# Optimization experiments

Measured on AMD Instinct MI355X. Metric: run time of the kernel, lower is better.

The kernel has to match this reference:

```python
import jax, jax.numpy as jnp
import numpy as np

EPS = 1e-12  # tf.nn.l2_normalize epsilon


def setup_inputs() -> dict:
    key = jax.random.key(0)
    k1, k2, k3 = jax.random.split(key, 3)
    T, NC, FW = 16384, 2048, 100
    x = jax.random.normal(k1, (T, NC), dtype=jnp.float32)
    weights = jax.random.normal(k2, (FW, NC), dtype=jnp.float32)
    biases = jax.random.normal(k3, (1, NC), dtype=jnp.float32)
    return {"x": x, "weights": weights, "biases": biases}


def reference(x, weights, biases):
    # x: [T, NC] (batch_size is the time axis), weights: [FW, NC], biases: [1, NC]
    FW, NC = weights.shape
    # pos_constraint then L2-normalize each filter along the lag axis
    w = jnp.maximum(weights, 0.0)
    w = w * jax.lax.rsqrt(jnp.maximum(jnp.sum(w * w, axis=0, keepdims=True), EPS))
    # The original pads the filter with FW trailing zeros and runs a SAME conv2d
    # over a [NC, T, 1, 1] input, then takes diag_part to recover the per-channel
    # result. With kernel size 2*FW, SAME pads (FW-1) above / FW below; the FW
    # trailing zero taps never contribute, so this equals a cross-correlation
    # with left padding FW-1: out[t, c] = sum_k w[k, c] * x[t + k - (FW-1), c].
    xT = x.T[None]                 # [1, NC, T]
    kern = w.T[:, None, :]         # [NC, 1, FW] depthwise kernel (OIH)
    pre = jax.lax.conv_general_dilated(
        xT, kern,
        window_strides=(1,),
        padding=[(FW - 1, 0)],
        dimension_numbers=("NCH", "OIH", "NCH"),
        feature_group_count=NC,
    )                              # [1, NC, T]
    pre = pre[0].T + biases        # [T, NC]
    return pre  # activation_func='lin' -> identity
```

## Files before the change

### kernel.cpp

```cpp
#include <hip/hip_runtime.h>


#define T_TOT 16384
#define NCH   2048
#define FW    100
#define CB    32
#define TB    128
#define RING  256
#define MROWS 24
#define BROWS (RING + MROWS)
#define NTHR  256
#define TTH   16
#define UK    10
#define NKC   (FW / UK)
#define NSEG  12
#define NCHUNK_TOT (T_TOT / TB)

__global__ __launch_bounds__(NTHR)
void catent_fir(const float* __restrict__ x,
                const float* __restrict__ wraw,
                const float* __restrict__ bias,
                float* __restrict__ out) {
    __shared__ float ring[BROWS * CB];
    __shared__ float wlds[FW * CB];
    __shared__ float scl[CB];

    const int tid   = threadIdx.x;
    const int cgrp  = blockIdx.x & 63;
    const int sidx  = blockIdx.x >> 6;
    const int cbase = cgrp * CB;

    const int ch0 = (sidx * NCHUNK_TOT) / NSEG;
    const int ch1 = ((sidx + 1) * NCHUNK_TOT) / NSEG;
    const int tseg0 = ch0 * TB;

    for (int i = tid; i < FW * CB; i += NTHR) {
        int k = i >> 5, c = i & 31;
        wlds[i] = fmaxf(wraw[(size_t)k * NCH + cbase + c], 0.0f);
    }
    __syncthreads();
    if (tid < CB) {
        float s = 0.0f;
        #pragma unroll 4
        for (int k = 0; k < FW; ++k) { float v = wlds[k * CB + tid]; s = fmaf(v, v, s); }
        scl[tid] = rsqrtf(fmaxf(s, 1e-12f));
    }
    __syncthreads();
    for (int i = tid; i < FW * CB; i += NTHR) wlds[i] *= scl[i & 31];

    for (int p = 0; p < 8; ++p) {
        int idx = tid + p * NTHR;
        int row = idx >> 3;
        int c4  = (idx & 7) * 4;
        int t   = tseg0 - TB + row;
        float4 v = make_float4(0.f, 0.f, 0.f, 0.f);
        if (t >= 0) v = *reinterpret_cast<const float4*>(&x[(size_t)t * NCH + cbase + c4]);
        int r = t & (RING - 1);
        *reinterpret_cast<float4*>(&ring[r * CB + c4]) = v;
        if (r < MROWS)
            *reinterpret_cast<float4*>(&ring[(RING + r) * CB + c4]) = v;
    }
    __syncthreads();

    const int c = tid & 31;
    const int g = tid >> 5;
    const float biasr = bias[cbase + c];

    const int r0  = tid >> 3;
    const int sc4 = (tid & 7) * 4;

    for (int ch = ch0; ch < ch1; ++ch) {
        const int t0 = ch * TB;
        const bool do_stage = (ch + 1 < ch1);

        float4 st[4];
        if (do_stage) {
            const size_t gb = (size_t)(t0 + TB) * NCH + cbase + sc4;
            #pragma unroll
            for (int p = 0; p < 4; ++p)
                st[p] = *reinterpret_cast<const float4*>(&x[gb + (size_t)(r0 + p * 32) * NCH]);
        }

        float acc[TTH];
        #pragma unroll
        for (int i = 0; i < TTH; ++i) acc[i] = biasr;

        const int rowbase0 = t0 - (FW - 1) + g * TTH;
        #pragma unroll 1
        for (int kc = 0; kc < NKC; ++kc) {
            const int br = (rowbase0 + kc * UK) & (RING - 1);
            const float* xb = &ring[br * CB + c];
            const float* wb = &wlds[(kc * UK) * CB + c];
            float wk[UK];
            #pragma unroll
            for (int u = 0; u < UK; ++u) wk[u] = wb[u * CB];
            float xj[TTH + UK - 1];
            #pragma unroll
            for (int j = 0; j < TTH + UK - 1; ++j) xj[j] = xb[j * CB];
            #pragma unroll
            for (int u = 0; u < UK; ++u)
                #pragma unroll
                for (int t = 0; t < TTH; ++t)
                    acc[t] = fmaf(wk[u], xj[t + u], acc[t]);
        }

        {
            size_t ob = (size_t)(t0 + g * TTH) * NCH + cbase + c;
            #pragma unroll
            for (int t = 0; t < TTH; ++t) out[ob + (size_t)t * NCH] = acc[t];
        }

        __syncthreads();

        if (do_stage) {
            const int rbase = (t0 + TB) & (RING - 1);
            #pragma unroll
            for (int p = 0; p < 4; ++p) {
                int r = rbase + r0 + p * 32;
                *reinterpret_cast<float4*>(&ring[r * CB + sc4]) = st[p];
                if (r < MROWS)
                    *reinterpret_cast<float4*>(&ring[(RING + r) * CB + sc4]) = st[p];
            }
        }
        __syncthreads();
    }
}

extern "C" void kernel_launch(void* const* d_in, const int* in_sizes, int n_in,
                              void* d_out, int out_size, void* d_ws, size_t ws_size,
                              hipStream_t stream) {
    const float* x    = (const float*)d_in[0];
    const float* wraw = (const float*)d_in[1];
    const float* bias = (const float*)d_in[2];
    float* out = (float*)d_out;

    dim3 grid(64 * NSEG);
    dim3 block(NTHR);
    catent_fir<<<grid, block, 0, stream>>>(x, wraw, bias, out);
}
```

Before: 130.1 us.

## Transpose LDS ring to channel-major rows with float4 reads and rotating register window

Stores the x ring buffer and weights in LDS as channel-major rows (padded row lengths 292/108) so each thread reads its channel's time samples with float4 loads. The tap loop becomes a rotating 24-entry register window, one 8-tap phase at a time, so each 8 new samples are reused across 16 outputs. Weights get a leading zero pad so the taps line up with 8-aligned sample reads, and output stores move after the staging barrier. In exchange, the global loads for staging become scalar per-channel loads instead of float4, and register pressure rises.

Result: faster. 111.6 us (-14.2%).

```diff
diff --git a/kernel.cpp b/kernel.cpp
--- a/kernel.cpp
+++ b/kernel.cpp
@@ -6,23 +6,40 @@
 #define FW    100
 #define CB    32
 #define TB    128
-#define RING  256
-#define MROWS 24
-#define BROWS (RING + MROWS)
 #define NTHR  256
 #define TTH   16
-#define UK    10
-#define NKC   (FW / UK)
+#define ROWL  292
+#define WROW  108
 #define NSEG  12
 #define NCHUNK_TOT (T_TOT / TB)
+
+#define KC_PHASE(PH, NS) do {                                                   \
+    int ro_ = tk & 255;                                                         \
+    float4 n0_ = *(const float4*)(rrow + ro_);                                  \
+    float4 n1_ = *(const float4*)(rrow + ro_ + 4);                              \
+    float4 w0_ = *(const float4*)(wp);                                          \
+    float4 w1_ = *(const float4*)(wp + 4);                                      \
+    float wk_[8];                                                               \
+    wk_[0]=w0_.x; wk_[1]=w0_.y; wk_[2]=w0_.z; wk_[3]=w0_.w;                     \
+    wk_[4]=w1_.x; wk_[5]=w1_.y; wk_[6]=w1_.z; wk_[7]=w1_.w;                     \
+    xw[(NS)+0]=n0_.x; xw[(NS)+1]=n0_.y; xw[(NS)+2]=n0_.z; xw[(NS)+3]=n0_.w;     \
+    xw[(NS)+4]=n1_.x; xw[(NS)+5]=n1_.y; xw[(NS)+6]=n1_.z; xw[(NS)+7]=n1_.w;     \
+    _Pragma("unroll")                                                           \
+    for (int u_ = 0; u_ < 8; ++u_) {                                            \
+      _Pragma("unroll")                                                         \
+      for (int i_ = 0; i_ < 16; ++i_)                                           \
+        acc[i_] = fmaf(wk_[u_], xw[((PH) + u_ + i_) % 24], acc[i_]);            \
+    }                                                                           \
+    tk += 8; wp += 8;                                                           \
+} while (0)
 
 __global__ __launch_bounds__(NTHR)
 void catent_fir(const float* __restrict__ x,
                 const float* __restrict__ wraw,
                 const float* __restrict__ bias,
                 float* __restrict__ out) {
-    __shared__ float ring[BROWS * CB];
-    __shared__ float wlds[FW * CB];
+    __shared__ float ring[CB * ROWL];
+    __shared__ float wl[CB * WROW];
     __shared__ float scl[CB];
 
     const int tid   = threadIdx.x;
@@ -34,95 +51,125 @@
     const int ch1 = ((sidx + 1) * NCHUNK_TOT) / NSEG;
     const int tseg0 = ch0 * TB;
 
+    const int c = tid & 31;
+    const int g = tid >> 5;
+
     for (int i = tid; i < FW * CB; i += NTHR) {
-        int k = i >> 5, c = i & 31;
-        wlds[i] = fmaxf(wraw[(size_t)k * NCH + cbase + c], 0.0f);
+        int k = i >> 5, cc = i & 31;
+        wl[cc * WROW + k + 1] = fmaxf(wraw[(size_t)k * NCH + cbase + cc], 0.0f);
+    }
+    if (tid < CB) {
+        wl[tid * WROW + 0] = 0.0f;
+        for (int j = FW + 1; j < WROW; ++j) wl[tid * WROW + j] = 0.0f;
     }
     __syncthreads();
     if (tid < CB) {
         float s = 0.0f;
         #pragma unroll 4
-        for (int k = 0; k < FW; ++k) { float v = wlds[k * CB + tid]; s = fmaf(v, v, s); }
+        for (int k = 1; k <= FW; ++k) { float v = wl[tid * WROW + k]; s = fmaf(v, v, s); }
         scl[tid] = rsqrtf(fmaxf(s, 1e-12f));
     }
     __syncthreads();
-    for (int i = tid; i < FW * CB; i += NTHR) wlds[i] *= scl[i & 31];
+    for (int i = tid; i < FW * CB; i += NTHR) {
+        int k = i >> 5, cc = i & 31;
+        wl[cc * WROW + k + 1] *= scl[cc];
+    }
 
-    for (int p = 0; p < 8; ++p) {
-        int idx = tid + p * NTHR;
-        int row = idx >> 3;
-        int c4  = (idx & 7) * 4;
-        int t   = tseg0 - TB + row;
-        float4 v = make_float4(0.f, 0.f, 0.f, 0.f);
-        if (t >= 0) v = *reinterpret_cast<const float4*>(&x[(size_t)t * NCH + cbase + c4]);
-        int r = t & (RING - 1);
-        *reinterpret_cast<float4*>(&ring[r * CB + c4]) = v;
-        if (r < MROWS)
-            *reinterpret_cast<float4*>(&ring[(RING + r) * CB + c4]) = v;
+    {
+        float* rw = &ring[c * ROWL];
+        for (int p = 0; p < 2; ++p) {
+            int tbase = tseg0 - TB + p * TB + g * 16;
+            float v[16];
+            #pragma unroll
+            for (int j = 0; j < 16; ++j) {
+                int t = tbase + j;
+                v[j] = (t >= 0) ? x[(size_t)t * NCH + cbase + c] : 0.0f;
+            }
+            int rm = tbase & 255;
+            #pragma unroll
+            for (int q = 0; q < 4; ++q)
+                *(float4*)(rw + rm + q * 4) = make_float4(v[q*4], v[q*4+1], v[q*4+2], v[q*4+3]);
+            if (rm < 32) {
+                #pragma unroll
+                for (int q = 0; q < 4; ++q)
+                    *(float4*)(rw + 256 + rm + q * 4) = make_float4(v[q*4], v[q*4+1], v[q*4+2], v[q*4+3]);
+            }
+        }
     }
     __syncthreads();
 
-    const int c = tid & 31;
-    const int g = tid >> 5;
     const float biasr = bias[cbase + c];
-
-    const int r0  = tid >> 3;
-    const int sc4 = (tid & 7) * 4;
+    const float* rrow = &ring[c * ROWL];
+    const float* wrow = &wl[c * WROW];
+    float* rwr = &ring[c * ROWL];
 
     for (int ch = ch0; ch < ch1; ++ch) {
         const int t0 = ch * TB;
         const bool do_stage = (ch + 1 < ch1);
 
-        float4 st[4];
+        float stv[16];
         if (do_stage) {
-            const size_t gb = (size_t)(t0 + TB) * NCH + cbase + sc4;
+            const size_t gb = (size_t)(t0 + TB + g * 16) * NCH + cbase + c;
             #pragma unroll
-            for (int p = 0; p < 4; ++p)
-                st[p] = *reinterpret_cast<const float4*>(&x[gb + (size_t)(r0 + p * 32) * NCH]);
+            for (int j = 0; j < 16; ++j) stv[j] = x[gb + (size_t)j * NCH];
         }
 
-        float acc[TTH];
+        float acc[16];
         #pragma unroll
-        for (int i = 0; i < TTH; ++i) acc[i] = biasr;
+        for (int i = 0; i < 16; ++i) acc[i] = biasr;
 
-        const int rowbase0 = t0 - (FW - 1) + g * TTH;
-        #pragma unroll 1
-        for (int kc = 0; kc < NKC; ++kc) {
-            const int br = (rowbase0 + kc * UK) & (RING - 1);
-            const float* xb = &ring[br * CB + c];
-            const float* wb = &wlds[(kc * UK) * CB + c];
-            float wk[UK];
+        float xw[24];
+        const int base0 = t0 + g * 16 - 100;
+
+        {
+            int ro = base0 & 255;
             #pragma unroll
-            for (int u = 0; u < UK; ++u) wk[u] = wb[u * CB];
-            float xj[TTH + UK - 1];
+            for (int q = 0; q < 6; ++q) {
+                float4 v = *(const float4*)(rrow + ro + q * 4);
+                xw[q*4+0] = v.x; xw[q*4+1] = v.y; xw[q*4+2] = v.z; xw[q*4+3] = v.w;
+            }
+            float4 w0 = *(const float4*)(wrow);
+            float4 w1 = *(const float4*)(wrow + 4);
+            float wk[8];
+            wk[0]=w0.x; wk[1]=w0.y; wk[2]=w0.z; wk[3]=w0.w;
+            wk[4]=w1.x; wk[5]=w1.y; wk[6]=w1.z; wk[7]=w1.w;
             #pragma unroll
-            for (int j = 0; j < TTH + UK - 1; ++j) xj[j] = xb[j * CB];
-            #pragma unroll
-            for (int u = 0; u < UK; ++u)
+            for (int u = 0; u < 8; ++u) {
                 #pragma unroll
-                for (int t = 0; t < TTH; ++t)
-                    acc[t] = fmaf(wk[u], xj[t + u], acc[t]);
+                for (int i = 0; i < 16; ++i)
+                    acc[i] = fmaf(wk[u], xw[(u + i) % 24], acc[i]);
+            }
         }
 
-        {
-            size_t ob = (size_t)(t0 + g * TTH) * NCH + cbase + c;
-            #pragma unroll
-            for (int t = 0; t < TTH; ++t) out[ob + (size_t)t * NCH] = acc[t];
+        int tk = base0 + 24;
+        const float* wp = wrow + 8;
+        #pragma unroll 1
+        for (int m = 0; m < 4; ++m) {
+            KC_PHASE(8, 0);
+            KC_PHASE(16, 8);
+            KC_PHASE(0, 16);
         }
 
         __syncthreads();
 
         if (do_stage) {
-            const int rbase = (t0 + TB) & (RING - 1);
+            int rm = (t0 + TB + g * 16) & 255;
             #pragma unroll
-            for (int p = 0; p < 4; ++p) {
-                int r = rbase + r0 + p * 32;
-                *reinterpret_cast<float4*>(&ring[r * CB + sc4]) = st[p];
-                if (r < MROWS)
-                    *reinterpret_cast<float4*>(&ring[(RING + r) * CB + sc4]) = st[p];
+            for (int q = 0; q < 4; ++q)
+                *(float4*)(rwr + rm + q * 4) = make_float4(stv[q*4], stv[q*4+1], stv[q*4+2], stv[q*4+3]);
+            if (rm < 32) {
+                #pragma unroll
+                for (int q = 0; q < 4; ++q)
+                    *(float4*)(rwr + 256 + rm + q * 4) = make_float4(stv[q*4], stv[q*4+1], stv[q*4+2], stv[q*4+3]);
             }
         }
         __syncthreads();
+
+        {
+            size_t ob = (size_t)(t0 + g * 16) * NCH + cbase + c;
+            #pragma unroll
+            for (int i = 0; i < 16; ++i) out[ob + (size_t)i * NCH] = acc[i];
+        }
     }
 }
 
```
